# Optimization experiments

Hardware: AMD Instinct MI355X
Metric: run time of the kernel (lower is better)

Reference implementation:

```python
import jax, jax.numpy as jnp
import numpy as np
from jax import lax

B, N, T, S, P, PM, H, K, PRED, L, HEADS = 32, 5, 20, 4, 2, 8, 64, 3, 40, 6, 4
D = H * T          # decoder d_model = hidden_dim * history_len = 1280
DFF = 2 * D        # decoder ffn multiplier = 2
DH = D // HEADS
SUB = 10           # rk4 step_size = 0.1 -> 10 substeps per unit of obs time


def setup_inputs() -> dict:
    key = jax.random.key(0)
    kit = iter(jax.random.split(key, 50))
    def g(shape, s=0.05):
        return jax.random.normal(next(kit), shape, dtype=jnp.float32) * s
    z = lambda shape: jnp.zeros(shape, jnp.float32)
    o = lambda shape: jnp.ones(shape, jnp.float32)
    return dict(
        data=g((B, N, T, S), 1.0),
        phy_params=g((B, PM), 1.0),
        Wi1=g((K, S + P + PM, H)), bi1=z((K, H)), Wi2=g((K, H, H)), bi2=z((K, H)),
        Wo1=g((H + S, H)), bo1=z((H,)), Wo2=g((H, H)), bo2=z((H,)),
        We1=g((S, H)), be1=z((H,)), We2=g((H, H)), be2=z((H,)),
        Wf=g((2 * H, H)), bf=z((H,)),
        Wg1=g((K, H, H)), bg1=z((K, H)), Wg2=g((K, H, H)), bg2=z((K, H)),
        Wq=g((L, D, D)), bq=z((L, D)), Wk=g((L, D, D)), bk=z((L, D)),
        Wv=g((L, D, D)), bv=z((L, D)), Woa=g((L, D, D)), boa=z((L, D)),
        ln1s=o((L, D)), ln1b=z((L, D)), ln2s=o((L, D)), ln2b=z((L, D)),
        Wff1=g((L, D, DFF)), bff1=z((L, DFF)), Wff2=g((L, DFF, D)), bff2=z((L, D)),
        Wout=g((D, S * PRED)), bout=z((S * PRED,)),
    )


def _ln(x, s, b):
    m = x.mean(-1, keepdims=True)
    v = ((x - m) ** 2).mean(-1, keepdims=True)
    return (x - m) * lax.rsqrt(v + 1e-5) * s + b


def reference(data, phy_params, Wi1, bi1, Wi2, bi2, Wo1, bo1, Wo2, bo2,
              We1, be1, We2, be2, Wf, bf, Wg1, bg1, Wg2, bg2,
              Wq, bq, Wk, bk, Wv, bv, Woa, boa, ln1s, ln1b, ln2s, ln2b,
              Wff1, bff1, Wff2, bff2, Wout, bout):
    # ---- per-prompt initializers: MLP on [state, pos, broadcast phy params] ----
    init_state = data[:, :, 0, :]                              # [B,N,S]
    init_pos = init_state[..., :P]
    pp = jnp.broadcast_to(phy_params[:, None, :], (B, N, PM))
    pin = jnp.concatenate([init_state, init_pos, pp], -1)      # [B,N,S+P+PM]
    h1 = jnp.tanh(jnp.einsum('bnf,kfh->kbnh', pin, Wi1) + bi1[:, None, None, :])
    z0 = jnp.einsum('kbnh,khg->kbng', h1, Wi2) + bi2[:, None, None, :]
    z0 = z0.reshape(K * B, N, H)

    obs = jnp.tile(data, (K, 1, 1, 1))                         # [K*B,N,T,S] (K clones)

    # ---- ODEFunc with linear interpolation of observations at time t ----
    def interp(t):
        i0 = jnp.clip(jnp.floor(t).astype(jnp.int32), 0, T - 2)
        w = t - i0.astype(jnp.float32)
        return (1.0 - w) * jnp.take(obs, i0, axis=2) + w * jnp.take(obs, i0 + 1, axis=2)

    def f(t, zz):
        hh = jnp.tanh(jnp.concatenate([zz, interp(t)], -1) @ Wo1 + bo1)
        return hh @ Wo2 + bo2

    hstep = 0.1
    def rk4(zz, t):
        k1 = f(t, zz)
        k2 = f(t + 0.5 * hstep, zz + 0.5 * hstep * k1)
        k3 = f(t + 0.5 * hstep, zz + 0.5 * hstep * k2)
        k4 = f(t + hstep, zz + hstep * k3)
        zn = zz + (hstep / 6.0) * (k1 + 2.0 * k2 + 2.0 * k3 + k4)
        return zn, zn

    ts = jnp.arange((T - 1) * SUB, dtype=jnp.float32) * hstep
    _, traj = lax.scan(rk4, z0, ts)
    traj = jnp.concatenate([z0[None], traj], 0)                # [(T-1)*SUB+1, K*B,N,H]
    z_t = jnp.transpose(traj[::SUB], (1, 2, 0, 3))             # [K*B,N,T,H]
    last_z = z_t[:, :, -1, :]

    # ---- backbone encoder (per-step MLP) ----
    mu = jnp.maximum(obs @ We1 + be1, 0.0) @ We2 + be2         # [K*B,N,T,H]
    last_mu = mu[:, :, -1, :]

    # ---- fusion + per-prompt gating ----
    proj = jnp.concatenate([z_t, mu], -1) @ Wf + bf            # [K*B,N,T,H]
    pk = proj.reshape(K, B, N, T, H)
    gh = jnp.tanh(jnp.einsum('kbnth,khg->kbntg', pk, Wg1) + bg1[:, None, None, None, :])
    gate = jax.nn.sigmoid(jnp.einsum('kbnth,khg->kbntg', gh, Wg2) + bg2[:, None, None, None, :])
    x = (pk * gate).reshape(K * B, N, T * H)                   # [K*B,N,D]

    # ---- backbone decoder: post-LN transformer over the N particles ----
    scale = 1.0 / float(DH) ** 0.5
    def layer(xx, p):
        wq, bq_, wk, bk_, wv, bv_, wo, bo_, l1s, l1b, l2s, l2b, w1, b1, w2, b2 = p
        q = (xx @ wq + bq_).reshape(K * B, N, HEADS, DH)
        kk = (xx @ wk + bk_).reshape(K * B, N, HEADS, DH)
        vv = (xx @ wv + bv_).reshape(K * B, N, HEADS, DH)
        att = jax.nn.softmax(jnp.einsum('bqhd,bkhd->bhqk', q, kk) * scale, axis=-1)
        o_ = jnp.einsum('bhqk,bkhd->bqhd', att, vv).reshape(K * B, N, D)
        xx = _ln(xx + o_ @ wo + bo_, l1s, l1b)
        xx = _ln(xx + jnp.maximum(xx @ w1 + b1, 0.0) @ w2 + b2, l2s, l2b)
        return xx, None

    x, _ = lax.scan(layer, x, (Wq, bq, Wk, bk, Wv, bv, Woa, boa,
                               ln1s, ln1b, ln2s, ln2b, Wff1, bff1, Wff2, bff2))
    pred = (x @ Wout + bout).reshape(K, B, N, PRED, S)
    return pred, last_mu.reshape(K, B, N, H), last_z.reshape(K, B, N, H)
```

## Files before the change

### kernel.cpp

```cpp
#include <hip/hip_runtime.h>
#include <hip/hip_bf16.h>


using bf16 = __hip_bfloat16;
typedef unsigned short u16;
typedef __bf16 bf16x8 __attribute__((ext_vector_type(8)));
typedef float f32x4 __attribute__((ext_vector_type(4)));

#define DEV_INLINE __device__ __forceinline__

DEV_INLINE bf16 f2bf(float v) { return __float2bfloat16(v); }
DEV_INLINE u16 f2bfu(float v) {
  bf16 h = __float2bfloat16(v);
  return *(u16*)&h;
}
DEV_INLINE float rlf(float v, int lane) {
  return __uint_as_float(__builtin_amdgcn_readlane(__float_as_uint(v), lane));
}
DEV_INLINE float ftanh(float x) {
  float ax = fminf(fabsf(x), 15.f);
  float e = __expf(-2.f * ax);
  float r = (1.f - e) * __builtin_amdgcn_rcpf(1.f + e);
  return x < 0.f ? -r : r;
}
DEV_INLINE float fsig(float x) {
  return __builtin_amdgcn_rcpf(1.f + __expf(-x));
}

constexpr size_t SLICE_DD = 1280 * 1280;
constexpr size_t SLICE_DF = 1280 * 2560;
constexpr size_t WT_Q   = 0;
constexpr size_t WT_K   = SLICE_DD;
constexpr size_t WT_V   = 2 * SLICE_DD;
constexpr size_t WT_O   = 3 * SLICE_DD;
constexpr size_t WT_F1  = 4 * SLICE_DD;
constexpr size_t WT_F2  = WT_F1 + SLICE_DF;
constexpr size_t WT_OUT = WT_F2 + SLICE_DF;
constexpr size_t WT_END = WT_OUT + 160 * 1280;
constexpr size_t FOFF   = WT_END * 2;
constexpr size_t F_ZT = 0;
constexpr size_t F_XF = F_ZT + 614400;
constexpr size_t F_Q  = F_XF + 614400;
constexpr size_t F_K  = F_Q + 614400;
constexpr size_t F_V  = F_K + 614400;
constexpr size_t F_T1 = F_V + 614400;
constexpr size_t F_END = F_T1 + 1228800;
constexpr size_t HOFF = FOFF + F_END * 4;
constexpr size_t H_XH = 0;
constexpr size_t H_OH = 614400;
constexpr size_t H_FF = 1228800;

__global__ __launch_bounds__(256) void transpose_layer_kernel(
    const float* __restrict__ Wq, const float* __restrict__ Wk,
    const float* __restrict__ Wv, const float* __restrict__ Wo,
    const float* __restrict__ Wff1, const float* __restrict__ Wff2,
    const float* __restrict__ Wout, u16* __restrict__ wt, int l) {
  int bid = blockIdx.x;
  const float* src;
  u16* dst;
  int R, C, tile;
  if (bid < 6400) {
    int mat = bid / 1600;
    tile = bid % 1600;
    src = (mat == 0 ? Wq : mat == 1 ? Wk : mat == 2 ? Wv : Wo) + (size_t)l * SLICE_DD;
    dst = wt + (size_t)mat * SLICE_DD;
    R = 1280; C = 1280;
  } else if (bid < 9600) {
    tile = bid - 6400;
    src = Wff1 + (size_t)l * SLICE_DF;
    dst = wt + WT_F1;
    R = 1280; C = 2560;
  } else if (bid < 12800) {
    tile = bid - 9600;
    src = Wff2 + (size_t)l * SLICE_DF;
    dst = wt + WT_F2;
    R = 2560; C = 1280;
  } else {
    tile = bid - 12800;
    src = Wout;
    dst = wt + WT_OUT;
    R = 1280; C = 160;
  }
  int tc = C >> 5;
  int r0 = (tile / tc) << 5, c0 = (tile % tc) << 5;
  __shared__ u16 tl[32][36];
  int t = threadIdx.x;
  int rr = t >> 3, c4 = (t & 7) << 2;
  float4 v = *(const float4*)&src[(size_t)(r0 + rr) * C + (c0 + c4)];
  tl[rr][c4 + 0] = f2bfu(v.x);
  tl[rr][c4 + 1] = f2bfu(v.y);
  tl[rr][c4 + 2] = f2bfu(v.z);
  tl[rr][c4 + 3] = f2bfu(v.w);
  __syncthreads();
  ushort4 o;
  o.x = tl[c4 + 0][rr];
  o.y = tl[c4 + 1][rr];
  o.z = tl[c4 + 2][rr];
  o.w = tl[c4 + 3][rr];
  *(ushort4*)&dst[(size_t)(c0 + rr) * R + (r0 + c4)] = o;
}

template <int EPI>
__global__ __launch_bounds__(256) void gemm_bt(
    const u16* __restrict__ A, const u16* __restrict__ Bt, size_t btz,
    const float* __restrict__ bz0, const float* __restrict__ bz1,
    const float* __restrict__ bz2, float* __restrict__ Cf,
    bf16* __restrict__ Ch, size_t outz, int M, int N, int K) {
  const int tid = threadIdx.x;
  const int l = tid & 63;
  const int wn = tid >> 6;
  const int n0 = blockIdx.x * 128, m0 = blockIdx.y * 64;
  const int z = blockIdx.z;
  Bt += (size_t)z * btz;
  const float* bias = (z == 0) ? bz0 : (z == 1 ? bz1 : bz2);
  if (EPI == 0) Cf += (size_t)z * outz; else Ch += (size_t)z * outz;

  __shared__ u16 As[64 * 32];
  __shared__ u16 Bs[128 * 32];
  f32x4 acc[4][2] = {};

  const int oA = (tid & 3) * 8;
  int gr = m0 + (tid >> 2); if (gr >= M) gr = M - 1;
  int gn0 = n0 + (tid >> 2); if (gn0 >= N) gn0 = N - 1;
  int gn1 = n0 + 64 + (tid >> 2); if (gn1 >= N) gn1 = N - 1;
  const u16* pA  = &A[(size_t)gr * K + oA];
  const u16* pB0 = &Bt[(size_t)gn0 * K + oA];
  const u16* pB1 = &Bt[(size_t)gn1 * K + oA];

  uint4 va  = *(const uint4*)pA;
  uint4 vb0 = *(const uint4*)pB0;
  uint4 vb1 = *(const uint4*)pB1;

  for (int kt = 0; kt < K; kt += 32) {
    __syncthreads();
    *(uint4*)&As[tid * 8] = va;
    *(uint4*)&Bs[tid * 8] = vb0;
    *(uint4*)&Bs[(tid + 256) * 8] = vb1;
    __syncthreads();
    if (kt + 32 < K) {
      va  = *(const uint4*)(pA + kt + 32);
      vb0 = *(const uint4*)(pB0 + kt + 32);
      vb1 = *(const uint4*)(pB1 + kt + 32);
    }
    bf16x8 af[4], bfr[2];
#pragma unroll
    for (int mt = 0; mt < 4; mt++)
      af[mt] = *(const bf16x8*)&As[(mt * 16 + (l & 15)) * 32 + (l >> 4) * 8];
#pragma unroll
    for (int nt = 0; nt < 2; nt++)
      bfr[nt] = *(const bf16x8*)&Bs[(wn * 32 + nt * 16 + (l & 15)) * 32 + (l >> 4) * 8];
#pragma unroll
    for (int mt = 0; mt < 4; mt++)
#pragma unroll
      for (int nt = 0; nt < 2; nt++)
        acc[mt][nt] = __builtin_amdgcn_mfma_f32_16x16x32_bf16(af[mt], bfr[nt], acc[mt][nt], 0, 0, 0);
  }

#pragma unroll
  for (int mt = 0; mt < 4; mt++)
#pragma unroll
    for (int nt = 0; nt < 2; nt++)
#pragma unroll
      for (int r = 0; r < 4; r++) {
        int row = m0 + mt * 16 + (l >> 4) * 4 + r;
        int col = n0 + wn * 32 + nt * 16 + (l & 15);
        if (row < M && col < N) {
          float v = acc[mt][nt][r] + bias[col];
          if (EPI == 1) v = fmaxf(v, 0.f);
          if (EPI == 0) Cf[(size_t)row * N + col] = v;
          else Ch[(size_t)row * N + col] = f2bf(v);
        }
      }
}

__global__ __launch_bounds__(64) void ode_kernel(
    const float* __restrict__ data, const float* __restrict__ phy,
    const float* __restrict__ Wi1, const float* __restrict__ bi1,
    const float* __restrict__ Wi2, const float* __restrict__ bi2,
    const float* __restrict__ Wo1, const float* __restrict__ bo1,
    const float* __restrict__ Wo2, const float* __restrict__ bo2,
    float* __restrict__ z_t, float* __restrict__ out_z) {
  const int r = blockIdx.x;
  const int kb = r / 5, n = r % 5;
  const int kx = kb >> 5, b = kb & 31;
  const int lane = threadIdx.x;

  __shared__ float obs[80];
  obs[lane] = data[(size_t)(b * 5 + n) * 80 + lane];
  if (lane < 16) obs[64 + lane] = data[(size_t)(b * 5 + n) * 80 + 64 + lane];

  float w1[64], wx[4], w2[64];
#pragma unroll
  for (int i = 0; i < 64; i++) w1[i] = Wo1[i * 64 + lane];
#pragma unroll
  for (int s = 0; s < 4; s++) wx[s] = Wo1[(64 + s) * 64 + lane];
#pragma unroll
  for (int i = 0; i < 64; i++) w2[i] = Wo2[i * 64 + lane];
  const float bb1 = bo1[lane], bb2 = bo2[lane];

  __syncthreads();

  float pin[14];
#pragma unroll
  for (int s = 0; s < 4; s++) pin[s] = obs[s];
  pin[4] = obs[0];
  pin[5] = obs[1];
#pragma unroll
  for (int s = 0; s < 8; s++) pin[6 + s] = phy[b * 8 + s];

  float h1 = bi1[kx * 64 + lane];
#pragma unroll
  for (int f = 0; f < 14; f++)
    h1 = fmaf(pin[f], Wi1[(kx * 14 + f) * 64 + lane], h1);
  h1 = ftanh(h1);

  float zz = bi2[kx * 64 + lane];
#pragma unroll
  for (int i = 0; i < 64; i++)
    zz = fmaf(rlf(h1, i), Wi2[(size_t)(kx * 64 + i) * 64 + lane], zz);

  z_t[(size_t)r * 1280 + lane] = zz;

  auto feval = [&](float y, const float* o4) -> float {
    float a0 = 0.f, a1 = 0.f, a2 = 0.f, a3 = 0.f;
#pragma unroll
    for (int i = 0; i < 64; i += 4) {
      a0 = fmaf(rlf(y, i + 0), w1[i + 0], a0);
      a1 = fmaf(rlf(y, i + 1), w1[i + 1], a1);
      a2 = fmaf(rlf(y, i + 2), w1[i + 2], a2);
      a3 = fmaf(rlf(y, i + 3), w1[i + 3], a3);
    }
    float hh = ((a0 + a1) + (a2 + a3)) + bb1;
#pragma unroll
    for (int s = 0; s < 4; s++) hh = fmaf(o4[s], wx[s], hh);
    hh = ftanh(hh);
    float q0 = 0.f, q1 = 0.f, q2 = 0.f, q3 = 0.f;
#pragma unroll
    for (int i = 0; i < 64; i += 4) {
      q0 = fmaf(rlf(hh, i + 0), w2[i + 0], q0);
      q1 = fmaf(rlf(hh, i + 1), w2[i + 1], q1);
      q2 = fmaf(rlf(hh, i + 2), w2[i + 2], q2);
      q3 = fmaf(rlf(hh, i + 3), w2[i + 3], q3);
    }
    return ((q0 + q1) + (q2 + q3)) + bb2;
  };

  auto interp4 = [&](float t, float* o) {
    int i0 = (int)t;
    if (i0 > 18) i0 = 18;
    float fr = t - (float)i0;
#pragma unroll
    for (int s = 0; s < 4; s++) {
      float a = obs[i0 * 4 + s], c = obs[i0 * 4 + 4 + s];
      o[s] = fmaf(fr, c - a, a);
    }
  };

  for (int j = 0; j < 190; j++) {
    float t = (float)j * 0.1f;
    float oA[4], oB[4], oC[4];
    interp4(t, oA);
    interp4(t + 0.05f, oB);
    interp4(t + 0.1f, oC);
    float k1 = feval(zz, oA);
    float k2 = feval(fmaf(0.05f, k1, zz), oB);
    float k3 = feval(fmaf(0.05f, k2, zz), oB);
    float k4 = feval(fmaf(0.1f, k3, zz), oC);
    zz = fmaf(0.1f / 6.f, k1 + 2.f * k2 + 2.f * k3 + k4, zz);
    if (((j + 1) % 10) == 0) {
      int tt = (j + 1) / 10;
      z_t[(size_t)(r * 20 + tt) * 64 + lane] = zz;
      if (tt == 19) out_z[(size_t)r * 64 + lane] = zz;
    }
  }
}

__global__ __launch_bounds__(64) void cd_kernel(
    const float* __restrict__ data, const float* __restrict__ z_t,
    const float* __restrict__ We1, const float* __restrict__ be1,
    const float* __restrict__ We2, const float* __restrict__ be2,
    const float* __restrict__ Wfm, const float* __restrict__ bfm,
    const float* __restrict__ Wg1, const float* __restrict__ bg1,
    const float* __restrict__ Wg2, const float* __restrict__ bg2,
    float* __restrict__ xf, bf16* __restrict__ xh, float* __restrict__ out_mu) {
  const int rt = blockIdx.x;
  const int lane = threadIdx.x;
  const int kb = rt / 100;
  const int rem = rt % 100;
  const int n = rem / 20, t = rem % 20;
  const int b = kb & 31, kx = kb >> 5;

  float obs4[4];
#pragma unroll
  for (int s = 0; s < 4; s++)
    obs4[s] = data[(size_t)((b * 5 + n) * 20 + t) * 4 + s];

  float mh = be1[lane];
#pragma unroll
  for (int s = 0; s < 4; s++) mh = fmaf(obs4[s], We1[s * 64 + lane], mh);
  mh = fmaxf(mh, 0.f);

  float mu = be2[lane];
#pragma unroll 16
  for (int h = 0; h < 64; h++) mu = fmaf(rlf(mh, h), We2[h * 64 + lane], mu);

  if (t == 19) out_mu[(size_t)(kb * 5 + n) * 64 + lane] = mu;

  float zv = z_t[(size_t)rt * 64 + lane];

  float pj = bfm[lane];
#pragma unroll 16
  for (int h = 0; h < 64; h++) pj = fmaf(rlf(zv, h), Wfm[h * 64 + lane], pj);
#pragma unroll 16
  for (int h = 0; h < 64; h++) pj = fmaf(rlf(mu, h), Wfm[(64 + h) * 64 + lane], pj);

  float gh = bg1[kx * 64 + lane];
#pragma unroll 16
  for (int h = 0; h < 64; h++)
    gh = fmaf(rlf(pj, h), Wg1[(size_t)(kx * 64 + h) * 64 + lane], gh);
  gh = ftanh(gh);

  float gt = bg2[kx * 64 + lane];
#pragma unroll 16
  for (int h = 0; h < 64; h++)
    gt = fmaf(rlf(gh, h), Wg2[(size_t)(kx * 64 + h) * 64 + lane], gt);
  gt = fsig(gt);

  float xv = pj * gt;
  size_t xo = (size_t)(kb * 5 + n) * 1280 + t * 64 + lane;
  xf[xo] = xv;
  xh[xo] = f2bf(xv);
}

__global__ __launch_bounds__(64) void attn_kernel(
    const float* __restrict__ q, const float* __restrict__ k,
    const float* __restrict__ v, bf16* __restrict__ oh) {
  const int kb = blockIdx.x >> 2, h = blockIdx.x & 3;
  const int lane = threadIdx.x;
  const size_t base = (size_t)(kb * 5) * 1280 + h * 320 + lane;
  float qv[5][5], kv[5][5], vv[5][5];
#pragma unroll
  for (int i = 0; i < 5; i++)
#pragma unroll
    for (int c = 0; c < 5; c++) {
      size_t off = base + (size_t)i * 1280 + c * 64;
      qv[i][c] = q[off];
      kv[i][c] = k[off];
      vv[i][c] = v[off];
    }
  float s[5][5];
#pragma unroll
  for (int i = 0; i < 5; i++)
#pragma unroll
    for (int j = 0; j < 5; j++) {
      float a = 0.f;
#pragma unroll
      for (int c = 0; c < 5; c++) a = fmaf(qv[i][c], kv[j][c], a);
#pragma unroll
      for (int m = 1; m < 64; m <<= 1) a += __shfl_xor(a, m, 64);
      s[i][j] = a * 0.055901699437494745f;
    }
#pragma unroll
  for (int i = 0; i < 5; i++) {
    float mx = s[i][0];
#pragma unroll
    for (int j = 1; j < 5; j++) mx = fmaxf(mx, s[i][j]);
    float sum = 0.f;
#pragma unroll
    for (int j = 0; j < 5; j++) {
      s[i][j] = __expf(s[i][j] - mx);
      sum += s[i][j];
    }
    float inv = __builtin_amdgcn_rcpf(sum);
#pragma unroll
    for (int j = 0; j < 5; j++) s[i][j] *= inv;
  }
#pragma unroll
  for (int i = 0; i < 5; i++)
#pragma unroll
    for (int c = 0; c < 5; c++) {
      float a = 0.f;
#pragma unroll
      for (int j = 0; j < 5; j++) a = fmaf(s[i][j], vv[j][c], a);
      oh[base + (size_t)i * 1280 + c * 64] = f2bf(a);
    }
}

__global__ __launch_bounds__(256) void ln_kernel(
    const float* __restrict__ g, float* __restrict__ xf, bf16* __restrict__ xh,
    const float* __restrict__ sc, const float* __restrict__ bi) {
  const int row = blockIdx.x, tid = threadIdx.x;
  const size_t base = (size_t)row * 1280;
  float v[5], s1 = 0.f, s2 = 0.f;
#pragma unroll
  for (int i = 0; i < 5; i++) {
    int c = tid + i * 256;
    float x = xf[base + c] + g[base + c];
    v[i] = x;
    s1 += x;
    s2 = fmaf(x, x, s2);
  }
#pragma unroll
  for (int m = 1; m < 64; m <<= 1) {
    s1 += __shfl_xor(s1, m, 64);
    s2 += __shfl_xor(s2, m, 64);
  }
  __shared__ float r1[4], r2[4];
  const int wv = tid >> 6;
  if ((tid & 63) == 0) { r1[wv] = s1; r2[wv] = s2; }
  __syncthreads();
  s1 = r1[0] + r1[1] + r1[2] + r1[3];
  s2 = r2[0] + r2[1] + r2[2] + r2[3];
  const float mean = s1 * (1.f / 1280.f);
  float var = s2 * (1.f / 1280.f) - mean * mean;
  var = fmaxf(var, 0.f);
  const float rs = rsqrtf(var + 1e-5f);
#pragma unroll
  for (int i = 0; i < 5; i++) {
    int c = tid + i * 256;
    float y = (v[i] - mean) * rs * sc[c] + bi[c];
    xf[base + c] = y;
    xh[base + c] = f2bf(y);
  }
}

extern "C" void kernel_launch(void* const* d_in, const int* in_sizes, int n_in,
                              void* d_out, int out_size, void* d_ws, size_t ws_size,
                              hipStream_t stream) {
  const float* data = (const float*)d_in[0];
  const float* phy  = (const float*)d_in[1];
  const float* Wi1  = (const float*)d_in[2];
  const float* bi1  = (const float*)d_in[3];
  const float* Wi2  = (const float*)d_in[4];
  const float* bi2  = (const float*)d_in[5];
  const float* Wo1  = (const float*)d_in[6];
  const float* bo1  = (const float*)d_in[7];
  const float* Wo2  = (const float*)d_in[8];
  const float* bo2  = (const float*)d_in[9];
  const float* We1  = (const float*)d_in[10];
  const float* be1  = (const float*)d_in[11];
  const float* We2  = (const float*)d_in[12];
  const float* be2  = (const float*)d_in[13];
  const float* Wfm  = (const float*)d_in[14];
  const float* bfm  = (const float*)d_in[15];
  const float* Wg1  = (const float*)d_in[16];
  const float* bg1  = (const float*)d_in[17];
  const float* Wg2  = (const float*)d_in[18];
  const float* bg2  = (const float*)d_in[19];
  const float* Wq   = (const float*)d_in[20];
  const float* bq   = (const float*)d_in[21];
  const float* Wk   = (const float*)d_in[22];
  const float* bk   = (const float*)d_in[23];
  const float* Wv   = (const float*)d_in[24];
  const float* bv   = (const float*)d_in[25];
  const float* Woa  = (const float*)d_in[26];
  const float* boa  = (const float*)d_in[27];
  const float* ln1s = (const float*)d_in[28];
  const float* ln1b = (const float*)d_in[29];
  const float* ln2s = (const float*)d_in[30];
  const float* ln2b = (const float*)d_in[31];
  const float* Wff1 = (const float*)d_in[32];
  const float* bff1 = (const float*)d_in[33];
  const float* Wff2 = (const float*)d_in[34];
  const float* bff2 = (const float*)d_in[35];
  const float* Wout = (const float*)d_in[36];
  const float* bout = (const float*)d_in[37];

  char* ws = (char*)d_ws;
  u16* wt = (u16*)ws;
  float* fb  = (float*)(ws + FOFF);
  float* z_t = fb + F_ZT;
  float* xf  = fb + F_XF;
  float* fq  = fb + F_Q;
  float* fk  = fb + F_K;
  float* fv  = fb + F_V;
  float* t1  = fb + F_T1;
  bf16* hb  = (bf16*)(ws + HOFF);
  bf16* xh  = hb + H_XH;
  bf16* oh  = hb + H_OH;
  bf16* ffh = hb + H_FF;

  float* out = (float*)d_out;
  float* out_pred = out;
  float* out_mu   = out + 76800;
  float* out_z    = out + 107520;

  ode_kernel<<<480, 64, 0, stream>>>(data, phy, Wi1, bi1, Wi2, bi2,
                                     Wo1, bo1, Wo2, bo2, z_t, out_z);
  cd_kernel<<<9600, 64, 0, stream>>>(data, z_t, We1, be1, We2, be2,
                                     Wfm, bfm, Wg1, bg1, Wg2, bg2,
                                     xf, xh, out_mu);

  for (int l = 0; l < 6; l++) {
    transpose_layer_kernel<<<13000, 256, 0, stream>>>(
        Wq, Wk, Wv, Woa, Wff1, Wff2, Wout, wt, l);
    gemm_bt<0><<<dim3(10, 8, 3), 256, 0, stream>>>(
        (const u16*)xh, wt + WT_Q, SLICE_DD,
        bq + l * 1280, bk + l * 1280, bv + l * 1280,
        fq, nullptr, 614400, 480, 1280, 1280);
    attn_kernel<<<384, 64, 0, stream>>>(fq, fk, fv, oh);
    gemm_bt<0><<<dim3(10, 8, 1), 256, 0, stream>>>(
        (const u16*)oh, wt + WT_O, 0,
        boa + l * 1280, boa + l * 1280, boa + l * 1280,
        t1, nullptr, 0, 480, 1280, 1280);
    ln_kernel<<<480, 256, 0, stream>>>(t1, xf, xh, ln1s + l * 1280, ln1b + l * 1280);
    gemm_bt<1><<<dim3(20, 8, 1), 256, 0, stream>>>(
        (const u16*)xh, wt + WT_F1, 0,
        bff1 + l * 2560, bff1 + l * 2560, bff1 + l * 2560,
        nullptr, ffh, 0, 480, 2560, 1280);
    gemm_bt<0><<<dim3(10, 8, 1), 256, 0, stream>>>(
        (const u16*)ffh, wt + WT_F2, 0,
        bff2 + l * 1280, bff2 + l * 1280, bff2 + l * 1280,
        t1, nullptr, 0, 480, 1280, 2560);
    ln_kernel<<<480, 256, 0, stream>>>(t1, xf, xh, ln2s + l * 1280, ln2b + l * 1280);
  }

  gemm_bt<0><<<dim3(2, 8, 1), 256, 0, stream>>>(
      (const u16*)xh, wt + WT_OUT, 0, bout, bout, bout,
      out_pred, nullptr, 0, 480, 160, 1280);
}
```

Before: 1.493 ms.

## Double-buffer GEMM LDS tiles with a 64-wide K step and register prefetch

The bf16 GEMM now moves through K in steps of 64 instead of 32 and keeps two LDS buffers. Each iteration loads its MFMA fragments from the current buffer, stores the prefetched next tile into the other buffer, and issues global loads two tiles ahead, so there is one barrier per step instead of two. The ODE kernel also gets a launch_bounds minimum-blocks hint of 1, which may change register allocation. The change costs more LDS and registers, and it assumes K is a multiple of 64; any remainder would be silently dropped.

```diff
diff --git a/kernel.cpp b/kernel.cpp
--- a/kernel.cpp
+++ b/kernel.cpp
@@ -115,45 +115,81 @@
   const float* bias = (z == 0) ? bz0 : (z == 1 ? bz1 : bz2);
   if (EPI == 0) Cf += (size_t)z * outz; else Ch += (size_t)z * outz;
 
-  __shared__ u16 As[64 * 32];
-  __shared__ u16 Bs[128 * 32];
+  __shared__ u16 As[2][2][64 * 32];
+  __shared__ u16 Bs[2][2][128 * 32];
   f32x4 acc[4][2] = {};
 
-  const int oA = (tid & 3) * 8;
-  int gr = m0 + (tid >> 2); if (gr >= M) gr = M - 1;
-  int gn0 = n0 + (tid >> 2); if (gn0 >= N) gn0 = N - 1;
-  int gn1 = n0 + 64 + (tid >> 2); if (gn1 >= N) gn1 = N - 1;
-  const u16* pA  = &A[(size_t)gr * K + oA];
-  const u16* pB0 = &Bt[(size_t)gn0 * K + oA];
-  const u16* pB1 = &Bt[(size_t)gn1 * K + oA];
-
-  uint4 va  = *(const uint4*)pA;
-  uint4 vb0 = *(const uint4*)pB0;
-  uint4 vb1 = *(const uint4*)pB1;
-
-  for (int kt = 0; kt < K; kt += 32) {
+  const int lrow = tid >> 2;
+  const int loct = (tid & 3) * 8;
+  int ar  = m0 + lrow;      if (ar  >= M) ar  = M - 1;
+  int br0 = n0 + lrow;      if (br0 >= N) br0 = N - 1;
+  int br1 = n0 + 64 + lrow; if (br1 >= N) br1 = N - 1;
+  const u16* pA  = &A [(size_t)ar  * K + loct];
+  const u16* pB0 = &Bt[(size_t)br0 * K + loct];
+  const u16* pB1 = &Bt[(size_t)br1 * K + loct];
+
+  uint4 a0  = *(const uint4*)(pA);
+  uint4 a1  = *(const uint4*)(pA + 32);
+  uint4 b00 = *(const uint4*)(pB0);
+  uint4 b01 = *(const uint4*)(pB0 + 32);
+  uint4 b10 = *(const uint4*)(pB1);
+  uint4 b11 = *(const uint4*)(pB1 + 32);
+
+  *(uint4*)&As[0][0][tid * 8] = a0;
+  *(uint4*)&As[0][1][tid * 8] = a1;
+  *(uint4*)&Bs[0][0][tid * 8] = b00;
+  *(uint4*)&Bs[0][1][tid * 8] = b01;
+  *(uint4*)&Bs[0][0][(tid + 256) * 8] = b10;
+  *(uint4*)&Bs[0][1][(tid + 256) * 8] = b11;
+
+  const int nT = K >> 6;
+  if (nT > 1) {
+    a0  = *(const uint4*)(pA  + 64);
+    a1  = *(const uint4*)(pA  + 96);
+    b00 = *(const uint4*)(pB0 + 64);
+    b01 = *(const uint4*)(pB0 + 96);
+    b10 = *(const uint4*)(pB1 + 64);
+    b11 = *(const uint4*)(pB1 + 96);
+  }
+  __syncthreads();
+
+  for (int it = 0; it < nT; it++) {
+    const int p = it & 1;
+    bf16x8 af[2][4], bfr[2][2];
+#pragma unroll
+    for (int ks = 0; ks < 2; ks++) {
+#pragma unroll
+      for (int mt = 0; mt < 4; mt++)
+        af[ks][mt] = *(const bf16x8*)&As[p][ks][(mt * 16 + (l & 15)) * 32 + (l >> 4) * 8];
+#pragma unroll
+      for (int nt = 0; nt < 2; nt++)
+        bfr[ks][nt] = *(const bf16x8*)&Bs[p][ks][(wn * 32 + nt * 16 + (l & 15)) * 32 + (l >> 4) * 8];
+    }
+    if (it + 1 < nT) {
+      *(uint4*)&As[1 - p][0][tid * 8] = a0;
+      *(uint4*)&As[1 - p][1][tid * 8] = a1;
+      *(uint4*)&Bs[1 - p][0][tid * 8] = b00;
+      *(uint4*)&Bs[1 - p][1][tid * 8] = b01;
+      *(uint4*)&Bs[1 - p][0][(tid + 256) * 8] = b10;
+      *(uint4*)&Bs[1 - p][1][(tid + 256) * 8] = b11;
+      if (it + 2 < nT) {
+        const int off = (it + 2) * 64;
+        a0  = *(const uint4*)(pA  + off);
+        a1  = *(const uint4*)(pA  + off + 32);
+        b00 = *(const uint4*)(pB0 + off);
+        b01 = *(const uint4*)(pB0 + off + 32);
+        b10 = *(const uint4*)(pB1 + off);
+        b11 = *(const uint4*)(pB1 + off + 32);
+      }
+    }
+#pragma unroll
+    for (int ks = 0; ks < 2; ks++)
+#pragma unroll
+      for (int mt = 0; mt < 4; mt++)
+#pragma unroll
+        for (int nt = 0; nt < 2; nt++)
+          acc[mt][nt] = __builtin_amdgcn_mfma_f32_16x16x32_bf16(af[ks][mt], bfr[ks][nt], acc[mt][nt], 0, 0, 0);
     __syncthreads();
-    *(uint4*)&As[tid * 8] = va;
-    *(uint4*)&Bs[tid * 8] = vb0;
-    *(uint4*)&Bs[(tid + 256) * 8] = vb1;
-    __syncthreads();
-    if (kt + 32 < K) {
-      va  = *(const uint4*)(pA + kt + 32);
-      vb0 = *(const uint4*)(pB0 + kt + 32);
-      vb1 = *(const uint4*)(pB1 + kt + 32);
-    }
-    bf16x8 af[4], bfr[2];
-#pragma unroll
-    for (int mt = 0; mt < 4; mt++)
-      af[mt] = *(const bf16x8*)&As[(mt * 16 + (l & 15)) * 32 + (l >> 4) * 8];
-#pragma unroll
-    for (int nt = 0; nt < 2; nt++)
-      bfr[nt] = *(const bf16x8*)&Bs[(wn * 32 + nt * 16 + (l & 15)) * 32 + (l >> 4) * 8];
-#pragma unroll
-    for (int mt = 0; mt < 4; mt++)
-#pragma unroll
-      for (int nt = 0; nt < 2; nt++)
-        acc[mt][nt] = __builtin_amdgcn_mfma_f32_16x16x32_bf16(af[mt], bfr[nt], acc[mt][nt], 0, 0, 0);
   }
 
 #pragma unroll
@@ -173,7 +209,7 @@
       }
 }
 
-__global__ __launch_bounds__(64) void ode_kernel(
+__global__ __launch_bounds__(64, 1) void ode_kernel(
     const float* __restrict__ data, const float* __restrict__ phy,
     const float* __restrict__ Wi1, const float* __restrict__ bi1,
     const float* __restrict__ Wi2, const float* __restrict__ bi2,
```

Result: faster. 1.325 ms (-11.2%).
